# Kernel optimization log

Measured on AMD Instinct MI355X. Metric: run time of the kernel, lower is better.

## Reference

```python
import jax, jax.numpy as jnp
import numpy as np

NEG = -1e30  # effective -inf, safe under fp32


def setup_inputs() -> dict:
    key = jax.random.key(0)
    k1, k2, k3 = jax.random.split(key, 3)
    T, B, C, L = 2000, 512, 29, 150  # C = num_classes + num_replabels = 28 + 1
    inputs = jax.random.normal(k1, (T, B, C), dtype=jnp.float32)
    transitions = jax.random.normal(k2, (C + 1, C), dtype=jnp.float32) * 0.1
    targets = jax.random.randint(k3, (B, L), 0, C, dtype=jnp.int32)
    return {"inputs": inputs, "transitions": transitions, "targets": targets}


def _asg_loss(inputs, transitions, targets):
    # inputs: [T, B, C] unnormalized emissions (time-major, as fed to the module)
    # transitions: [C+1, C]; row 0 = start scores, transitions[1+c, p] = score(p -> c)
    # targets: [B, L] int labels (replabel-packed), values in [0, C)
    T, B, C = inputs.shape
    L = targets.shape[1]
    start = transitions[0]          # [C]
    trans = transitions[1:]         # [C, C]; trans[next, prev]

    # ---- denominator: log-sum-exp over all paths in the fully connected lattice ----
    alpha0 = inputs[0] + start[None, :]                                   # [B, C]
    def den_step(alpha, e_t):
        # alpha[b, p] -> logsumexp_p(alpha[b, p] + trans[c, p]) per next-class c
        a = jax.nn.logsumexp(alpha[:, None, :] + trans[None, :, :], axis=-1)
        return e_t + a, None
    alphaT, _ = jax.lax.scan(den_step, alpha0, inputs[1:])
    log_den = jax.nn.logsumexp(alphaT, axis=-1)                           # [B]

    # ---- numerator: forced alignment over the target chain with self-loops ----
    idx = jnp.broadcast_to(targets[None, :, :], (T, B, L))
    e_y = jnp.take_along_axis(inputs, idx, axis=2)                        # [T, B, L]
    stay_t = trans[targets, targets]                                      # [B, L] self-loop
    move_t = trans[targets[:, 1:], targets[:, :-1]]                       # [B, L-1] y_{l-1}->y_l
    move_t = jnp.concatenate([jnp.zeros((B, 1), inputs.dtype), move_t], axis=1)
    l_is0 = jnp.arange(L) == 0
    num0 = jnp.where(l_is0[None, :], start[targets[:, 0]][:, None] + e_y[0], NEG)
    def num_step(alpha, e_t):
        shifted = jnp.pad(alpha[:, :-1], ((0, 0), (1, 0)), constant_values=NEG)
        a = jnp.logaddexp(alpha + stay_t, shifted + move_t)
        return e_t + a, None
    alphaL, _ = jax.lax.scan(num_step, num0, e_y[1:])
    log_num = alphaL[:, -1]                                               # [B]

    # loss_b = logZ_full - logZ_forced_align; 'mean' reduction over batch
    return jnp.mean(log_den - log_num)


def reference(inputs, transitions, targets):
    return _asg_loss(inputs, transitions, targets)
```

## Files before the change

### kernel.cpp

```cpp
#include <hip/hip_runtime.h>

static constexpr int Tn = 2000;
static constexpr int Bn = 512;
static constexpr int Cn = 29;
static constexpr int Ln = 150;
static constexpr float LOG2E_F = 1.4426950408889634f;
static constexpr float LN2_F   = 0.6931471805599453f;
static constexpr float NEGV    = -1e30f;

static constexpr int WS_DEN_F = 0;
static constexpr int WS_NUM_F = 2 * 512 * 32;
static constexpr int WS_NUM_B = 2 * 512 * 32 + 512 * 160;

typedef float  f32x16 __attribute__((ext_vector_type(16)));
typedef float  f32x4  __attribute__((ext_vector_type(4)));
typedef __bf16 bf16x8 __attribute__((ext_vector_type(8)));
typedef unsigned int u32x4 __attribute__((ext_vector_type(4)));

#if __has_builtin(__builtin_amdgcn_exp2f)
#define FEXP2(x) __builtin_amdgcn_exp2f(x)
#else
#define FEXP2(x) exp2f(x)
#endif
#if __has_builtin(__builtin_amdgcn_logf)
#define FLOG2(x) __builtin_amdgcn_logf(x)
#else
#define FLOG2(x) log2f(x)
#endif

__device__ __forceinline__ float ladd2(float x, float y) {
    float m = fmaxf(x, y);
    float d = fminf(x, y) - m;
    return m + FLOG2(1.0f + FEXP2(d));
}
__device__ __forceinline__ int exp_of(float x) {
    return ((__float_as_int(x) >> 23) & 255) - 127;
}
__device__ __forceinline__ float pow2i(int e) {
    return __int_as_float((e + 127) << 23);
}
__device__ __forceinline__ unsigned short f2bf_rne(float x) {
    unsigned u = __float_as_uint(x);
    u += 0x7fffu + ((u >> 16) & 1u);
    return (unsigned short)(u >> 16);
}
__device__ __forceinline__ unsigned cvtpk_bf16(float lo, float hi) {
    unsigned r;
    asm("v_cvt_pk_bf16_f32 %0, %1, %2" : "=v"(r) : "v"(lo), "v"(hi));
    return r;
}
__device__ __forceinline__ void xswap32(unsigned &a, unsigned &b) {
#if __has_builtin(__builtin_amdgcn_permlane32_swap)
    auto r = __builtin_amdgcn_permlane32_swap(a, b, false, false);
    a = r[0]; b = r[1];
#else
    unsigned pa = (unsigned)__shfl_xor((int)a, 32);
    unsigned pb = (unsigned)__shfl_xor((int)b, 32);
    bool hb = (threadIdx.x & 32) != 0;
    unsigned na = hb ? pb : a;
    unsigned nb = hb ? b : pa;
    a = na; b = nb;
#endif
}
__device__ __forceinline__ void packDtoB(const float* W, bf16x8 &B1, bf16x8 &B2) {
    unsigned pk[8];
#pragma unroll
    for (int q = 0; q < 8; ++q) pk[q] = cvtpk_bf16(W[2 * q], W[2 * q + 1]);
    xswap32(pk[0], pk[2]); xswap32(pk[1], pk[3]);
    xswap32(pk[4], pk[6]); xswap32(pk[5], pk[7]);
    B1 = __builtin_bit_cast(bf16x8, u32x4{pk[0], pk[1], pk[2], pk[3]});
    B2 = __builtin_bit_cast(bf16x8, u32x4{pk[4], pk[5], pk[6], pk[7]});
}
__device__ __forceinline__ void renorm16(float* W, float &Sacc) {
    float m = W[0];
#pragma unroll
    for (int r = 1; r < 16; ++r) m = fmaxf(m, W[r]);
#pragma unroll
    for (int sh = 1; sh <= 32; sh <<= 1) m = fmaxf(m, __shfl_xor(m, sh));
    int g = exp_of(m);
    float iv = pow2i(-g);
#pragma unroll
    for (int r = 0; r < 16; ++r) W[r] *= iv;
    Sacc += (float)g;
}

__global__ __launch_bounds__(256, 4)
void asg_scan(const float* __restrict__ inp, const float* __restrict__ tr,
              const int* __restrict__ tg, float* __restrict__ ws)
{
    const int tid = threadIdx.x;
    const int bid = blockIdx.x;

    __shared__ float mats[4][32][33];
    __shared__ float uring[4][8][32];
    __shared__ float scl[4];

    if (bid < 512) {
        const int lane = tid & 63;
        const int wid  = tid >> 6;
        const int col  = lane & 31;
        const int hi   = lane >> 5;
        const int b    = bid;
        const size_t BC = (size_t)Bn * Cn;

        unsigned aw[8];
#pragma unroll
        for (int p = 0; p < 8; ++p) {
            int kb = (p >> 2) * 16 + 8 * hi + (p & 3) * 2;
            unsigned short lo = 0, hh = 0;
            if (col < Cn) {
                if (kb < Cn)     lo = f2bf_rne(FEXP2(LOG2E_F * tr[(1 + col) * Cn + kb]));
                if (kb + 1 < Cn) hh = f2bf_rne(FEXP2(LOG2E_F * tr[(1 + col) * Cn + kb + 1]));
            }
            aw[p] = (unsigned)lo | ((unsigned)hh << 16);
        }
        const bf16x8 A1 = __builtin_bit_cast(bf16x8, u32x4{aw[0], aw[1], aw[2], aw[3]});
        const bf16x8 A2 = __builtin_bit_cast(bf16x8, u32x4{aw[4], aw[5], aw[6], aw[7]});

        f32x16 z;
#pragma unroll
        for (int r = 0; r < 16; ++r) z[r] = 0.f;

        const int start = 1 + 500 * wid;
        const int cnt   = min(500, Tn - start);

        const float* ebase = inp + (size_t)b * Cn + min(col, Cn - 1);

        float er[8];
#pragma unroll
        for (int p = 0; p < 8; ++p)
            er[p] = ebase[(size_t)min(start + p, Tn - 1) * BC];

        if (lane < 32) {
            uring[wid][0][col] = FEXP2(LOG2E_F * er[0]);
            uring[wid][1][col] = FEXP2(LOG2E_F * er[1]);
        }

        float W[16];
#pragma unroll
        for (int r = 0; r < 16; ++r) {
            int row = (r & 3) + 8 * (r >> 2) + 4 * hi;
            W[r] = (row == col) ? 1.0f : 0.0f;
        }
        float Sacc = 0.f;

        int s = 0;
        for (; s + 8 <= cnt; s += 8) {
#pragma unroll
            for (int u = 0; u < 8; ++u) {
                er[u] = ebase[(size_t)min(start + s + u + 8, Tn - 1) * BC];
                float un = FEXP2(LOG2E_F * er[(u + 2) & 7]);
                if (lane < 32) uring[wid][(u + 2) & 7][col] = un;
                f32x4 uu0 = *(const f32x4*)&uring[wid][u][4 * hi];
                f32x4 uu1 = *(const f32x4*)&uring[wid][u][8 + 4 * hi];
                f32x4 uu2 = *(const f32x4*)&uring[wid][u][16 + 4 * hi];
                f32x4 uu3 = *(const f32x4*)&uring[wid][u][24 + 4 * hi];
                bf16x8 B1, B2;
                packDtoB(W, B1, B2);
                f32x16 d = __builtin_amdgcn_mfma_f32_32x32x16_bf16(A1, B1, z, 0, 0, 0);
                d = __builtin_amdgcn_mfma_f32_32x32x16_bf16(A2, B2, d, 0, 0, 0);
#pragma unroll
                for (int r = 0; r < 16; ++r) {
                    f32x4 uq = (r < 4) ? uu0 : (r < 8) ? uu1 : (r < 12) ? uu2 : uu3;
                    W[r] = d[r] * uq[r & 3];
                }
                if (u == 7) renorm16(W, Sacc);
            }
        }
        {
            const int rem = cnt - s;
            if (lane < 32) {
#pragma unroll
                for (int j = 2; j < 8; ++j)
                    if (j < rem) uring[wid][j][col] = FEXP2(LOG2E_F * er[j]);
            }
#pragma unroll
            for (int u = 0; u < 8; ++u) {
                if (u < rem) {
                    f32x4 uu0 = *(const f32x4*)&uring[wid][u][4 * hi];
                    f32x4 uu1 = *(const f32x4*)&uring[wid][u][8 + 4 * hi];
                    f32x4 uu2 = *(const f32x4*)&uring[wid][u][16 + 4 * hi];
                    f32x4 uu3 = *(const f32x4*)&uring[wid][u][24 + 4 * hi];
                    bf16x8 B1, B2;
                    packDtoB(W, B1, B2);
                    f32x16 d = __builtin_amdgcn_mfma_f32_32x32x16_bf16(A1, B1, z, 0, 0, 0);
                    d = __builtin_amdgcn_mfma_f32_32x32x16_bf16(A2, B2, d, 0, 0, 0);
#pragma unroll
                    for (int r = 0; r < 16; ++r) {
                        f32x4 uq = (r < 4) ? uu0 : (r < 8) ? uu1 : (r < 12) ? uu2 : uu3;
                        W[r] = d[r] * uq[r & 3];
                    }
                }
            }
            renorm16(W, Sacc);
        }

#pragma unroll
        for (int r = 0; r < 16; ++r) {
            int row = (r & 3) + 8 * (r >> 2) + 4 * hi;
            mats[wid][row][col] = W[r];
        }
        if (lane == 0) scl[wid] = Sacc;
        __syncthreads();

        f32x16 q = z;
        float Sq = 0.f;
        if (wid < 2) {
            const float (*Lm)[33] = mats[2 * wid + 1];
            const float (*Rm)[33] = mats[2 * wid];
            unsigned lw[8];
#pragma unroll
            for (int p = 0; p < 8; ++p) {
                int kb = (p >> 2) * 16 + 8 * hi + (p & 3) * 2;
                lw[p] = (unsigned)f2bf_rne(Lm[col][kb]) |
                        ((unsigned)f2bf_rne(Lm[col][kb + 1]) << 16);
            }
            bf16x8 LA1 = __builtin_bit_cast(bf16x8, u32x4{lw[0], lw[1], lw[2], lw[3]});
            bf16x8 LA2 = __builtin_bit_cast(bf16x8, u32x4{lw[4], lw[5], lw[6], lw[7]});
            float Wr[16];
#pragma unroll
            for (int r = 0; r < 16; ++r) {
                int row = (r & 3) + 8 * (r >> 2) + 4 * hi;
                Wr[r] = Rm[row][col];
            }
            bf16x8 B1, B2;
            packDtoB(Wr, B1, B2);
            q = __builtin_amdgcn_mfma_f32_32x32x16_bf16(LA1, B1, z, 0, 0, 0);
            q = __builtin_amdgcn_mfma_f32_32x32x16_bf16(LA2, B2, q, 0, 0, 0);
            float Wq[16];
#pragma unroll
            for (int r = 0; r < 16; ++r) Wq[r] = q[r];
            float Sg = scl[2 * wid] + scl[2 * wid + 1];
            renorm16(Wq, Sg);
#pragma unroll
            for (int r = 0; r < 16; ++r) q[r] = Wq[r];
            Sq = Sg;
        }
        __syncthreads();
        if (wid == 1) {
#pragma unroll
            for (int r = 0; r < 16; ++r) {
                int row = (r & 3) + 8 * (r >> 2) + 4 * hi;
                mats[3][row][col] = q[r];
            }
            if (lane == 0) scl[3] = Sq;
        }
        __syncthreads();

        if (wid == 0) {
            unsigned lw[8];
#pragma unroll
            for (int p = 0; p < 8; ++p) {
                int kb = (p >> 2) * 16 + 8 * hi + (p & 3) * 2;
                lw[p] = (unsigned)f2bf_rne(mats[3][col][kb]) |
                        ((unsigned)f2bf_rne(mats[3][col][kb + 1]) << 16);
            }
            bf16x8 LA1 = __builtin_bit_cast(bf16x8, u32x4{lw[0], lw[1], lw[2], lw[3]});
            bf16x8 LA2 = __builtin_bit_cast(bf16x8, u32x4{lw[4], lw[5], lw[6], lw[7]});
            float Wq[16];
#pragma unroll
            for (int r = 0; r < 16; ++r) Wq[r] = q[r];
            bf16x8 B1, B2;
            packDtoB(Wq, B1, B2);
            f32x16 d = __builtin_amdgcn_mfma_f32_32x32x16_bf16(LA1, B1, z, 0, 0, 0);
            d = __builtin_amdgcn_mfma_f32_32x32x16_bf16(LA2, B2, d, 0, 0, 0);
            const float Stot = Sq + scl[3];
            float a0v = 0.f;
            if (col < Cn)
                a0v = FEXP2(LOG2E_F * (inp[(size_t)b * Cn + col] + tr[col]));
            float ssum = 0.f;
#pragma unroll
            for (int r = 0; r < 16; ++r) ssum += d[r];
            float t = ssum * a0v;
#pragma unroll
            for (int sh = 1; sh <= 32; sh <<= 1) t += __shfl_xor(t, sh);
            if (lane == 0) ws[WS_DEN_F + b] = FLOG2(t) + Stot;
        }
    } else {
        const int nid = (bid - 512) * 4 + (tid >> 6);
        const int dir = nid >> 9;
        const int b   = nid & 511;
        const int k   = tid & 63;
        const int* tb = tg + b * Ln;

        const int l0 = 3 * k, l1 = 3 * k + 1, l2 = 3 * k + 2;
        const int t0i = (l0 < Ln) ? tb[l0] : 0;
        const int t1i = (l1 < Ln) ? tb[l1] : 0;
        const int t2i = (l2 < Ln) ? tb[l2] : 0;
        const float s0c = LOG2E_F * tr[(1 + t0i) * Cn + t0i];
        const float s1c = LOG2E_F * tr[(1 + t1i) * Cn + t1i];
        const float s2c = LOG2E_F * tr[(1 + t2i) * Cn + t2i];
        const int   p0  = (l0 >= 1 && l0 < Ln) ? tb[l0 - 1] : 0;
        const float m0c = (l0 >= 1 && l0 < Ln) ? LOG2E_F * tr[(1 + t0i) * Cn + p0] : 0.0f;
        const float m1c = (l1 < Ln) ? LOG2E_F * tr[(1 + t1i) * Cn + t0i] : 0.0f;
        const float m2c = (l2 < Ln) ? LOG2E_F * tr[(1 + t2i) * Cn + t1i] : 0.0f;

        float a0 = NEGV, a1 = NEGV, a2 = NEGV;
        if (dir == 0) {
            if (k == 0) a0 = LOG2E_F * (tr[t0i] + inp[(size_t)b * Cn + t0i]);
        } else {
            if (k == 49) a2 = 0.0f;
        }

        const int kk = (k < Cn) ? k : (Cn - 1);
        const float* eb = inp + (size_t)b * Cn + kk;
        const int t0    = dir ? (Tn - 1) : 1;
        const int dt    = dir ? -1 : 1;
        const int steps = dir ? 1000 : 999;

        float ce[8], ne[8];
#pragma unroll
        for (int u = 0; u < 8; ++u) {
            int tt = t0 + u * dt; tt = max(0, min(Tn - 1, tt));
            ce[u] = LOG2E_F * eb[(size_t)tt * (Bn * Cn)];
        }

        for (int s = 0; s < steps; s += 8) {
#pragma unroll
            for (int u = 0; u < 8; ++u) {
                int tt = t0 + (s + 8 + u) * dt; tt = max(0, min(Tn - 1, tt));
                ne[u] = LOG2E_F * eb[(size_t)tt * (Bn * Cn)];
            }
#pragma unroll
            for (int u = 0; u < 8; ++u) {
                if (s + u < steps) {
                    float rv = ce[u];
                    float e0  = __shfl(rv, t0i);
                    float e1  = __shfl(rv, t1i);
                    float eg2 = __shfl(rv, t2i);
                    if (dir == 0) {
                        float sh = __shfl_up(a2, 1);
                        sh = (k == 0) ? NEGV : sh;
                        float n0 = e0  + ladd2(a0 + s0c, sh + m0c);
                        float n1 = e1  + ladd2(a1 + s1c, a0 + m1c);
                        float n2 = eg2 + ladd2(a2 + s2c, a1 + m2c);
                        a0 = n0; a1 = n1; a2 = n2;
                    } else {
                        float sv0 = a0 + s0c + e0;
                        float mv0 = a0 + m0c + e0;
                        float sv1 = a1 + s1c + e1;
                        float mv1 = a1 + m1c + e1;
                        float sv2 = a2 + s2c + eg2;
                        float mv2 = a2 + m2c + eg2;
                        float mn = __shfl_down(mv0, 1);
                        mn = (k == 49) ? NEGV : mn;
                        a0 = ladd2(sv0, mv1);
                        a1 = ladd2(sv1, mv2);
                        a2 = ladd2(sv2, mn);
                    }
                }
            }
#pragma unroll
            for (int u = 0; u < 8; ++u) ce[u] = ne[u];
        }
        const int base = (dir ? WS_NUM_B : WS_NUM_F) + b * 160;
        if (l0 < Ln)     ws[base + l0]     = a0;
        if (l0 + 1 < Ln) ws[base + l0 + 1] = a1;
        if (l0 + 2 < Ln) ws[base + l0 + 2] = a2;
    }
}

__global__ __launch_bounds__(512)
void asg_combine(const float* __restrict__ ws, float* __restrict__ out)
{
    __shared__ float red[512];
    const int b = threadIdx.x;

    const float ld = ws[WS_DEN_F + b];

    const float* nf = ws + WS_NUM_F + b * 160;
    const float* nb = ws + WS_NUM_B + b * 160;
    float vm2 = -3.0e38f;
    for (int l = 0; l < Ln; ++l) vm2 = fmaxf(vm2, nf[l] + nb[l]);
    float sum2 = 0.f;
    for (int l = 0; l < Ln; ++l) sum2 += FEXP2(nf[l] + nb[l] - vm2);
    float ln = vm2 + FLOG2(sum2);

    red[b] = ld - ln;
    __syncthreads();
    for (int off = 256; off > 0; off >>= 1) {
        if (b < off) red[b] += red[b + off];
        __syncthreads();
    }
    if (b == 0) out[0] = red[0] * (LN2_F / 512.0f);
}

extern "C" void kernel_launch(void* const* d_in, const int* in_sizes, int n_in,
                              void* d_out, int out_size, void* d_ws, size_t ws_size,
                              hipStream_t stream)
{
    const float* inp = (const float*)d_in[0];
    const float* tr  = (const float*)d_in[1];
    const int*   tg  = (const int*)d_in[2];
    float* out = (float*)d_out;
    float* ws  = (float*)d_ws;

    hipLaunchKernelGGL(asg_scan,    dim3(768), dim3(256), 0, stream, inp, tr, tg, ws);
    hipLaunchKernelGGL(asg_combine, dim3(1),   dim3(512), 0, stream, ws, out);
}
```

Measured before the change: 273.1 us.

## Split denominator time scan into eight segments with tree-reduced matrix products

Each denominator block now uses 8 waves, each scanning 250 timesteps instead of 4 waves of 500, which halves the serial chain per wave. The segment transfer matrices are then combined through a three-level tree of MFMA products in LDS. Numerator blocks are moved to the front of the grid and pack 8 waves per 512-thread block. The cost is more LDS per block, lower occupancy bounds, and an extra reduction level that adds bf16 rounding.

```diff
diff --git a/kernel.cpp b/kernel.cpp
--- a/kernel.cpp
+++ b/kernel.cpp
@@ -11,6 +11,9 @@
 static constexpr int WS_DEN_F = 0;
 static constexpr int WS_NUM_F = 2 * 512 * 32;
 static constexpr int WS_NUM_B = 2 * 512 * 32 + 512 * 160;
+
+static constexpr int NSEG = 8;
+static constexpr int SEGL = 250;
 
 typedef float  f32x16 __attribute__((ext_vector_type(16)));
 typedef float  f32x4  __attribute__((ext_vector_type(4)));
@@ -84,23 +87,23 @@
     Sacc += (float)g;
 }
 
-__global__ __launch_bounds__(256, 4)
+__global__ __launch_bounds__(512)
 void asg_scan(const float* __restrict__ inp, const float* __restrict__ tr,
               const int* __restrict__ tg, float* __restrict__ ws)
 {
     const int tid = threadIdx.x;
     const int bid = blockIdx.x;
 
-    __shared__ float mats[4][32][33];
-    __shared__ float uring[4][8][32];
-    __shared__ float scl[4];
-
-    if (bid < 512) {
+    __shared__ float mats[NSEG][32][33];
+    __shared__ float uring[NSEG][8][32];
+    __shared__ float scl[NSEG];
+
+    if (bid >= 128) {
         const int lane = tid & 63;
         const int wid  = tid >> 6;
         const int col  = lane & 31;
         const int hi   = lane >> 5;
-        const int b    = bid;
+        const int b    = bid - 128;
         const size_t BC = (size_t)Bn * Cn;
 
         unsigned aw[8];
@@ -121,8 +124,8 @@
 #pragma unroll
         for (int r = 0; r < 16; ++r) z[r] = 0.f;
 
-        const int start = 1 + 500 * wid;
-        const int cnt   = min(500, Tn - start);
+        const int start = 1 + SEGL * wid;
+        const int cnt   = min(SEGL, Tn - start);
 
         const float* ebase = inp + (size_t)b * Cn + min(col, Cn - 1);
 
@@ -203,11 +206,7 @@
         if (lane == 0) scl[wid] = Sacc;
         __syncthreads();
 
-        f32x16 q = z;
-        float Sq = 0.f;
-        if (wid < 2) {
-            const float (*Lm)[33] = mats[2 * wid + 1];
-            const float (*Rm)[33] = mats[2 * wid];
+        auto lds_mul = [&](const float (*Lm)[33], const float (*Rm)[33], float* Wo) {
             unsigned lw[8];
 #pragma unroll
             for (int p = 0; p < 8; ++p) {
@@ -225,59 +224,54 @@
             }
             bf16x8 B1, B2;
             packDtoB(Wr, B1, B2);
-            q = __builtin_amdgcn_mfma_f32_32x32x16_bf16(LA1, B1, z, 0, 0, 0);
-            q = __builtin_amdgcn_mfma_f32_32x32x16_bf16(LA2, B2, q, 0, 0, 0);
+            f32x16 d = __builtin_amdgcn_mfma_f32_32x32x16_bf16(LA1, B1, z, 0, 0, 0);
+            d = __builtin_amdgcn_mfma_f32_32x32x16_bf16(LA2, B2, d, 0, 0, 0);
+#pragma unroll
+            for (int r = 0; r < 16; ++r) Wo[r] = d[r];
+        };
+        auto store_mat = [&](int slot, const float* Wo) {
+#pragma unroll
+            for (int r = 0; r < 16; ++r) {
+                int row = (r & 3) + 8 * (r >> 2) + 4 * hi;
+                mats[slot][row][col] = Wo[r];
+            }
+        };
+
+        if (wid < 4) {
             float Wq[16];
-#pragma unroll
-            for (int r = 0; r < 16; ++r) Wq[r] = q[r];
+            lds_mul(mats[2 * wid + 1], mats[2 * wid], Wq);
             float Sg = scl[2 * wid] + scl[2 * wid + 1];
             renorm16(Wq, Sg);
-#pragma unroll
-            for (int r = 0; r < 16; ++r) q[r] = Wq[r];
-            Sq = Sg;
+            store_mat(2 * wid, Wq);
+            if (lane == 0) scl[2 * wid] = Sg;
         }
         __syncthreads();
-        if (wid == 1) {
-#pragma unroll
-            for (int r = 0; r < 16; ++r) {
-                int row = (r & 3) + 8 * (r >> 2) + 4 * hi;
-                mats[3][row][col] = q[r];
-            }
-            if (lane == 0) scl[3] = Sq;
+        if (wid < 2) {
+            float Wq[16];
+            lds_mul(mats[4 * wid + 2], mats[4 * wid], Wq);
+            float Sg = scl[4 * wid] + scl[4 * wid + 2];
+            renorm16(Wq, Sg);
+            store_mat(4 * wid, Wq);
+            if (lane == 0) scl[4 * wid] = Sg;
         }
         __syncthreads();
-
         if (wid == 0) {
-            unsigned lw[8];
-#pragma unroll
-            for (int p = 0; p < 8; ++p) {
-                int kb = (p >> 2) * 16 + 8 * hi + (p & 3) * 2;
-                lw[p] = (unsigned)f2bf_rne(mats[3][col][kb]) |
-                        ((unsigned)f2bf_rne(mats[3][col][kb + 1]) << 16);
-            }
-            bf16x8 LA1 = __builtin_bit_cast(bf16x8, u32x4{lw[0], lw[1], lw[2], lw[3]});
-            bf16x8 LA2 = __builtin_bit_cast(bf16x8, u32x4{lw[4], lw[5], lw[6], lw[7]});
             float Wq[16];
-#pragma unroll
-            for (int r = 0; r < 16; ++r) Wq[r] = q[r];
-            bf16x8 B1, B2;
-            packDtoB(Wq, B1, B2);
-            f32x16 d = __builtin_amdgcn_mfma_f32_32x32x16_bf16(LA1, B1, z, 0, 0, 0);
-            d = __builtin_amdgcn_mfma_f32_32x32x16_bf16(LA2, B2, d, 0, 0, 0);
-            const float Stot = Sq + scl[3];
+            lds_mul(mats[4], mats[0], Wq);
+            const float Stot = scl[0] + scl[4];
             float a0v = 0.f;
             if (col < Cn)
                 a0v = FEXP2(LOG2E_F * (inp[(size_t)b * Cn + col] + tr[col]));
             float ssum = 0.f;
 #pragma unroll
-            for (int r = 0; r < 16; ++r) ssum += d[r];
+            for (int r = 0; r < 16; ++r) ssum += Wq[r];
             float t = ssum * a0v;
 #pragma unroll
             for (int sh = 1; sh <= 32; sh <<= 1) t += __shfl_xor(t, sh);
             if (lane == 0) ws[WS_DEN_F + b] = FLOG2(t) + Stot;
         }
     } else {
-        const int nid = (bid - 512) * 4 + (tid >> 6);
+        const int nid = bid * 8 + (tid >> 6);
         const int dir = nid >> 9;
         const int b   = nid & 511;
         const int k   = tid & 63;
@@ -395,6 +389,6 @@
     float* out = (float*)d_out;
     float* ws  = (float*)d_ws;
 
-    hipLaunchKernelGGL(asg_scan,    dim3(768), dim3(256), 0, stream, inp, tr, tg, ws);
+    hipLaunchKernelGGL(asg_scan,    dim3(640), dim3(512), 0, stream, inp, tr, tg, ws);
     hipLaunchKernelGGL(asg_combine, dim3(1),   dim3(512), 0, stream, ws, out);
 }
```

Measured after the change: 286.2 us. 4.8% more time.
